# Kernel optimization log

Measured on AMD Instinct MI355X. Metric: run time of the kernel, lower is better.

## Reference

```python
import jax, jax.numpy as jnp
import numpy as np

B, N, C = 4, 2048, 1024
H = 16
HD = C // H
SCALE = HD ** -0.5


def setup_inputs() -> dict:
    key = jax.random.key(0)
    ks = jax.random.split(key, 5)
    s = 0.02
    return {
        "x": jax.random.normal(ks[0], (B, N, C), dtype=jnp.float32),
        "w_qkv": jax.random.normal(ks[1], (C, 3 * C), dtype=jnp.float32) * s,
        "b_qkv": jnp.zeros((3 * C,), dtype=jnp.float32),
        "w_proj": jax.random.normal(ks[2], (C, C), dtype=jnp.float32) * s,
        "b_proj": jnp.zeros((C,), dtype=jnp.float32),
    }


def reference(x, w_qkv, b_qkv, w_proj, b_proj):
    b, n, c = x.shape
    qkv = x @ w_qkv + b_qkv                       # [b, n, 3c]
    qkv = qkv.reshape(b, n, 3, H, HD)
    qkv = jnp.transpose(qkv, (2, 0, 3, 1, 4))     # [3, b, h, n, hd]
    q, k, v = qkv[0], qkv[1], qkv[2]
    attn = jnp.einsum("bhqd,bhkd->bhqk", q, k) * SCALE
    attn = jax.nn.softmax(attn, axis=-1)
    out = jnp.einsum("bhqk,bhkd->bhqd", attn, v)  # [b, h, n, hd]
    out = jnp.transpose(out, (0, 2, 1, 3)).reshape(b, n, c)
    return out @ w_proj + b_proj
```

## Files before the change

kernel.cpp:

```cpp
#include <hip/hip_runtime.h>
#include <cstdint>
#include <cstddef>


typedef __attribute__((ext_vector_type(8))) short short8;
typedef __attribute__((ext_vector_type(4))) float f32x4;
typedef _Float16 half4 __attribute__((ext_vector_type(4)));

#if __has_builtin(__builtin_amdgcn_exp2f)
#define EXP2F(x) __builtin_amdgcn_exp2f(x)
#else
#define EXP2F(x) __expf((x) * 0.69314718056f)
#endif

__device__ __forceinline__ short f2bf(float x) {
  unsigned u = __builtin_bit_cast(unsigned, x);
  u += 0x7fffu + ((u >> 16) & 1u);
  return (short)(u >> 16);
}

__device__ __forceinline__ unsigned pkh(float a, float b) {
  auto h = __builtin_amdgcn_cvt_pkrtz(a, b);
  return __builtin_bit_cast(unsigned, h);
}

__device__ __forceinline__ void async16(const void* g, void* l) {
  __builtin_amdgcn_global_load_lds(
      (const __attribute__((address_space(1))) unsigned*)g,
      (__attribute__((address_space(3))) unsigned*)l, 16, 0, 0);
}

__device__ __forceinline__ void barrier_raw() {
  __asm__ volatile("" ::: "memory");
  __builtin_amdgcn_s_barrier();
  __asm__ volatile("" ::: "memory");
}


__global__ __launch_bounds__(256) void prep_kernel(
    const float* __restrict__ x, const float* __restrict__ w_qkv,
    const float* __restrict__ w_proj, short* __restrict__ xs,
    short* __restrict__ wqkvT, short* __restrict__ wprojT) {
  __shared__ float tile[32][33];
  const int bid = blockIdx.x, tid = threadIdx.x;
  if (bid < 4096) {
    int i = bid * 256 + tid;
    const float4* p = (const float4*)x + (size_t)i * 2;
    float4 a = p[0], b = p[1];
    short8 r;
    r[0] = f2bf(a.x); r[1] = f2bf(a.y); r[2] = f2bf(a.z); r[3] = f2bf(a.w);
    r[4] = f2bf(b.x); r[5] = f2bf(b.y); r[6] = f2bf(b.z); r[7] = f2bf(b.w);
    *((short8*)xs + i) = r;
    return;
  }
  const float* in;
  short* out;
  int N, bx, by;
  if (bid < 4096 + 3072) {
    int b = bid - 4096;
    in = w_qkv; out = wqkvT; N = 3072; bx = b % 96; by = b / 96;
  } else {
    int b = bid - 7168;
    in = w_proj; out = wprojT; N = 1024; bx = b & 31; by = b >> 5;
  }
  const int K = 1024;
  int n0 = bx * 32, k0 = by * 32;
  int tx = tid & 31, ty = tid >> 5;
  for (int r = ty; r < 32; r += 8)
    tile[r][tx] = in[(size_t)(k0 + r) * N + n0 + tx];
  __syncthreads();
  for (int r = ty; r < 32; r += 8)
    out[(size_t)(n0 + r) * K + k0 + tx] = f2bf(tile[tx][r]);
}


template <int BM, int BN, int MODE>
__global__ __launch_bounds__(256, 2) void gemm_kernel(
    const short* __restrict__ A, const short* __restrict__ Bt,
    const float* __restrict__ bias, int Nn,
    short* __restrict__ qb, short* __restrict__ kb, short* __restrict__ vtb,
    float* __restrict__ outp) {
  constexpr int K = 1024;
  constexpr int NT = K / 32;
  constexpr int MR = BM / 32, NR = BN / 32;
  constexpr int L = (BM + BN) / 64;
  __shared__ __align__(16) short Ts[3][(BM + BN) * 32];
  const int tid = threadIdx.x, wave = tid >> 6, lane = tid & 63;
  const int quad = lane >> 4, l16 = lane & 15;

  const unsigned bid = blockIdx.x + gridDim.x * blockIdx.y;
  const unsigned c = bid & 7u, j = bid >> 3;
  const unsigned MC = gridDim.y >> 3;
  const unsigned chunk = MC * 8u;
  const unsigned nc = j / chunk, rem = j - nc * chunk;
  const unsigned m_idx = c * MC + (rem >> 3);
  const unsigned n_idx = nc * 8u + (rem & 7u);
  const int m0 = (int)m_idx * BM, n0 = (int)n_idx * BN;

  const int wrow = (wave >> 1) * (BM / 2), wcol = (wave & 1) * (BN / 2);

  const int srow = tid >> 2;
  const int sch8 = (((tid & 3) ^ (srow & 3)) * 8);
  const short* Ag = A + (size_t)(m0 + srow) * K + sch8;
  const short* Bg = Bt + (size_t)(n0 + srow) * K + sch8;
  const int fq8 = ((quad ^ (l16 & 3)) * 8);

  f32x4 acc[MR][NR] = {};

  auto stage = [&](int b, int kt) {
    char* dst = (char*)Ts[b] + tid * 16;
#pragma unroll
    for (int i = 0; i < BM / 64; ++i)
      async16(Ag + (size_t)(i * 64) * K + kt * 32, dst + i * 4096);
#pragma unroll
    for (int i = 0; i < BN / 64; ++i)
      async16(Bg + (size_t)(i * 64) * K + kt * 32, dst + (BM / 64 + i) * 4096);
  };

  stage(0, 0);
  stage(1, 1);
  if constexpr (L == 6) asm volatile("s_waitcnt vmcnt(6)" ::: "memory");
  else                  asm volatile("s_waitcnt vmcnt(4)" ::: "memory");
  barrier_raw();

  int cb = 0, sb = 2;
  for (int t = 0; t < NT; ++t) {
    if (t + 2 < NT) stage(sb, t + 2);

    const short* Tb = Ts[cb];
    short8 af[MR], bf[NR];
#pragma unroll
    for (int mf = 0; mf < MR; ++mf)
      af[mf] = *(const short8*)&Tb[(wrow + mf * 16 + l16) * 32 + fq8];
#pragma unroll
    for (int nf = 0; nf < NR; ++nf)
      bf[nf] = *(const short8*)&Tb[(BM + wcol + nf * 16 + l16) * 32 + fq8];

    __builtin_amdgcn_s_setprio(1);
#pragma unroll
    for (int mf = 0; mf < MR; ++mf)
#pragma unroll
      for (int nf = 0; nf < NR; ++nf)
        acc[mf][nf] = __builtin_amdgcn_mfma_f32_16x16x32_bf16(
            af[mf], bf[nf], acc[mf][nf], 0, 0, 0);
    __builtin_amdgcn_s_setprio(0);

    if (t + 2 < NT) {
      if constexpr (L == 6) asm volatile("s_waitcnt vmcnt(6)" ::: "memory");
      else                  asm volatile("s_waitcnt vmcnt(4)" ::: "memory");
    } else {
      asm volatile("s_waitcnt vmcnt(0)" ::: "memory");
    }
    barrier_raw();
    cb = cb + 1; if (cb >= 3) cb -= 3;
    sb = sb + 1; if (sb >= 3) sb -= 3;
  }

  if (MODE == 0) {
#pragma unroll
    for (int mf = 0; mf < MR; ++mf) {
      int row0 = m0 + wrow + mf * 16 + quad * 4;
      int b = row0 >> 11, n = row0 & 2047;
#pragma unroll
      for (int nf = 0; nf < NR; ++nf) {
        int col = n0 + wcol + nf * 16 + l16;
        float bv = bias[col];
        float v0 = acc[mf][nf][0] + bv, v1 = acc[mf][nf][1] + bv;
        float v2 = acc[mf][nf][2] + bv, v3 = acc[mf][nf][3] + bv;
        int which = col >> 10;
        int h = (col >> 6) & 15;
        int d = col & 63;
        size_t bh = (size_t)(b * 16 + h);
        if (which == 0) {
          const float qs = 0.18033688f;
          size_t base = (bh * 2048 + n) * 64 + d;
          qb[base]       = f2bf(v0 * qs);
          qb[base + 64]  = f2bf(v1 * qs);
          qb[base + 128] = f2bf(v2 * qs);
          qb[base + 192] = f2bf(v3 * qs);
        } else if (which == 1) {
          size_t base = (bh * 2048 + n) * 64 + d;
          kb[base]       = f2bf(v0);
          kb[base + 64]  = f2bf(v1);
          kb[base + 128] = f2bf(v2);
          kb[base + 192] = f2bf(v3);
        } else {
          uint2 pk;
          pk.x = pkh(v0, v1);
          pk.y = pkh(v2, v3);
          *(uint2*)&vtb[(bh * 64 + d) * 2048 + n] = pk;
        }
      }
    }
  } else {
#pragma unroll
    for (int mf = 0; mf < MR; ++mf) {
      int row0 = m0 + wrow + mf * 16 + quad * 4;
#pragma unroll
      for (int nf = 0; nf < NR; ++nf) {
        int col = n0 + wcol + nf * 16 + l16;
        float bv = bias[col];
        outp[(size_t)row0 * Nn + col]       = acc[mf][nf][0] + bv;
        outp[(size_t)(row0 + 1) * Nn + col] = acc[mf][nf][1] + bv;
        outp[(size_t)(row0 + 2) * Nn + col] = acc[mf][nf][2] + bv;
        outp[(size_t)(row0 + 3) * Nn + col] = acc[mf][nf][3] + bv;
      }
    }
  }
}


__global__ __launch_bounds__(256, 4) void attn_kernel(
    const short* __restrict__ qb, const short* __restrict__ kb,
    const short* __restrict__ vtb, short* __restrict__ ob) {
  __shared__ __align__(16) short Ks[2][64 * 64];
  __shared__ __align__(16) short Vs[2][64 * 64];
  const int tid = threadIdx.x, wave = tid >> 6, lane = tid & 63;
  const int quad = lane >> 4, l16 = lane & 15;
  int nlin = blockIdx.x + blockIdx.y * 16;
  nlin = (nlin & 7) * 128 + (nlin >> 3);
  const int q0 = (nlin & 15) * 128;
  const int bh = nlin >> 4;
  const short* Qg = qb + (size_t)bh * (2048 * 64);
  const short* Kg = kb + (size_t)bh * (2048 * 64);
  const short* Vg = vtb + (size_t)bh * (64 * 2048);

  short8 qf[2][2];
#pragma unroll
  for (int qt = 0; qt < 2; ++qt)
#pragma unroll
    for (int kc = 0; kc < 2; ++kc)
      qf[qt][kc] = *(const short8*)
          &Qg[(size_t)(q0 + wave * 32 + qt * 16 + l16) * 64 + kc * 32 + quad * 8];

  const int str = lane >> 3;
  const int sgc = ((lane & 7) ^ (str & 7)) * 8;
  const int fsw = l16 & 7;
  const int c0 = wave * 2, c1 = wave * 2 + 1;

  async16(Kg + (size_t)(c0 * 8 + str) * 64 + sgc, (char*)Ks[0] + c0 * 1024);
  async16(Kg + (size_t)(c1 * 8 + str) * 64 + sgc, (char*)Ks[0] + c1 * 1024);
  async16(Vg + (size_t)(c0 * 8 + str) * 2048 + sgc, (char*)Vs[0] + c0 * 1024);
  async16(Vg + (size_t)(c1 * 8 + str) * 2048 + sgc, (char*)Vs[0] + c1 * 1024);

  const half4 vone = {(_Float16)1.f, (_Float16)1.f, (_Float16)1.f, (_Float16)1.f};
  const f32x4 fz = {};
  f32x4 oacc[2][4] = {};
  f32x4 lacc[2] = {};

  for (int t = 0; t < 32; ++t) {
    __syncthreads();

    int kvn = (t + 1) * 64;
    if (kvn < 2048) {
      char* kd = (char*)Ks[(t + 1) & 1];
      char* vd = (char*)Vs[(t + 1) & 1];
      async16(Kg + (size_t)(kvn + c0 * 8 + str) * 64 + sgc, kd + c0 * 1024);
      async16(Kg + (size_t)(kvn + c1 * 8 + str) * 64 + sgc, kd + c1 * 1024);
      async16(Vg + (size_t)(c0 * 8 + str) * 2048 + kvn + sgc, vd + c0 * 1024);
      async16(Vg + (size_t)(c1 * 8 + str) * 2048 + kvn + sgc, vd + c1 * 1024);
    }
    const short* Kst = Ks[t & 1];
    const short* Vst = Vs[t & 1];

    f32x4 sacc[2][4];
#pragma unroll
    for (int kc = 0; kc < 2; ++kc) {
      short8 kf[4];
#pragma unroll
      for (int kvt = 0; kvt < 4; ++kvt)
        kf[kvt] = *(const short8*)
            &Kst[(kvt * 16 + l16) * 64 + (((kc * 4 + quad) ^ fsw) << 3)];
#pragma unroll
      for (int kvt = 0; kvt < 4; ++kvt)
#pragma unroll
        for (int qt = 0; qt < 2; ++qt)
          sacc[qt][kvt] = __builtin_amdgcn_mfma_f32_16x16x32_bf16(
              kf[kvt], qf[qt][kc], kc == 0 ? fz : sacc[qt][kvt], 0, 0, 0);
    }

#pragma unroll
    for (int kvt = 0; kvt < 4; ++kvt) {
      const int vcol = (((kvt * 2 + (quad >> 1)) ^ fsw) << 3) + (quad & 1) * 4;
      uint2 vr[4];
#pragma unroll
      for (int nt = 0; nt < 4; ++nt)
        vr[nt] = *(const uint2*)&Vst[(nt * 16 + l16) * 64 + vcol];

      half4 pfr[2];
#pragma unroll
      for (int qt = 0; qt < 2; ++qt) {
        float p0 = EXP2F(sacc[qt][kvt][0]);
        float p1 = EXP2F(sacc[qt][kvt][1]);
        float p2 = EXP2F(sacc[qt][kvt][2]);
        float p3 = EXP2F(sacc[qt][kvt][3]);
        uint2 w;
        w.x = pkh(p0, p1);
        w.y = pkh(p2, p3);
        pfr[qt] = __builtin_bit_cast(half4, w);
      }
#pragma unroll
      for (int qt = 0; qt < 2; ++qt)
        lacc[qt] = __builtin_amdgcn_mfma_f32_16x16x16f16(
            pfr[qt], vone, lacc[qt], 0, 0, 0);
#pragma unroll
      for (int nt = 0; nt < 4; ++nt) {
        half4 vfr = __builtin_bit_cast(half4, vr[nt]);
#pragma unroll
        for (int qt = 0; qt < 2; ++qt)
          oacc[qt][nt] = __builtin_amdgcn_mfma_f32_16x16x16f16(
              pfr[qt], vfr, oacc[qt][nt], 0, 0, 0);
      }
    }
  }

  const int b = bh >> 4, h = bh & 15;
#pragma unroll
  for (int qt = 0; qt < 2; ++qt) {
    float inv0 = 1.f / lacc[qt][0], inv1 = 1.f / lacc[qt][1];
    float inv2 = 1.f / lacc[qt][2], inv3 = 1.f / lacc[qt][3];
#pragma unroll
    for (int nt = 0; nt < 4; ++nt) {
      int d = nt * 16 + l16;
      int qbase = q0 + wave * 32 + qt * 16 + quad * 4;
      size_t obase = ((size_t)(b * 2048 + qbase)) * 1024 + h * 64 + d;
      ob[obase]        = f2bf(oacc[qt][nt][0] * inv0);
      ob[obase + 1024] = f2bf(oacc[qt][nt][1] * inv1);
      ob[obase + 2048] = f2bf(oacc[qt][nt][2] * inv2);
      ob[obase + 3072] = f2bf(oacc[qt][nt][3] * inv3);
    }
  }
}


extern "C" void kernel_launch(void* const* d_in, const int* in_sizes, int n_in,
                              void* d_out, int out_size, void* d_ws, size_t ws_size,
                              hipStream_t stream) {
  const float* x      = (const float*)d_in[0];
  const float* w_qkv  = (const float*)d_in[1];
  const float* b_qkv  = (const float*)d_in[2];
  const float* w_proj = (const float*)d_in[3];
  const float* b_proj = (const float*)d_in[4];
  float* out = (float*)d_out;

  short* xs     = (short*)d_ws;
  short* wqkvT  = xs + (size_t)8192 * 1024;
  short* wprojT = wqkvT + (size_t)3072 * 1024;
  short* qb     = wprojT + (size_t)1024 * 1024;
  short* kb     = qb + (size_t)64 * 2048 * 64;
  short* vtb    = kb + (size_t)64 * 2048 * 64;
  short* aob    = vtb + (size_t)64 * 2048 * 64;

  prep_kernel<<<dim3(8192), 256, 0, stream>>>(x, w_qkv, w_proj,
                                              xs, wqkvT, wprojT);

  gemm_kernel<256, 128, 0><<<dim3(24, 32), 256, 0, stream>>>(
      xs, wqkvT, b_qkv, 3072, qb, kb, vtb, nullptr);
  attn_kernel<<<dim3(16, 64), 256, 0, stream>>>(qb, kb, vtb, aob);
  gemm_kernel<128, 128, 1><<<dim3(8, 64), 256, 0, stream>>>(
      aob, wprojT, b_proj, 1024, nullptr, nullptr, nullptr, out);
}
```

Measured before the change: 267.1 us.

## Switch attention kernel to 32x32 MFMA tiles with permlane32 P-fragment swap

Rewrites the attention inner loop to use 32x32x16 MFMA instructions for both QK^T and PV, so each wave holds 32 query rows in lane-indexed layout. The softmax row sum is now accumulated directly in registers instead of through an extra MFMA against a ones vector. The P fragments are rearranged across wave halves with permlane32_swap, and s_setprio is raised around the PV MFMAs. This aims to cut MFMA instruction count, LDS reads and the redundant sum MFMAs, at the cost of a more complex register layout and a cross-lane shuffle.

```diff
diff --git a/kernel.cpp b/kernel.cpp
--- a/kernel.cpp
+++ b/kernel.cpp
@@ -5,7 +5,9 @@
 
 typedef __attribute__((ext_vector_type(8))) short short8;
 typedef __attribute__((ext_vector_type(4))) float f32x4;
-typedef _Float16 half4 __attribute__((ext_vector_type(4)));
+typedef __attribute__((ext_vector_type(16))) float f32x16;
+typedef _Float16 half8 __attribute__((ext_vector_type(8)));
+typedef __attribute__((ext_vector_type(2))) int iv2;
 
 #if __has_builtin(__builtin_amdgcn_exp2f)
 #define EXP2F(x) __builtin_amdgcn_exp2f(x)
@@ -216,7 +218,7 @@
   __shared__ __align__(16) short Ks[2][64 * 64];
   __shared__ __align__(16) short Vs[2][64 * 64];
   const int tid = threadIdx.x, wave = tid >> 6, lane = tid & 63;
-  const int quad = lane >> 4, l16 = lane & 15;
+  const int l31 = lane & 31, hi = lane >> 5;
   int nlin = blockIdx.x + blockIdx.y * 16;
   nlin = (nlin & 7) * 128 + (nlin >> 3);
   const int q0 = (nlin & 15) * 128;
@@ -225,17 +227,14 @@
   const short* Kg = kb + (size_t)bh * (2048 * 64);
   const short* Vg = vtb + (size_t)bh * (64 * 2048);
 
-  short8 qf[2][2];
-#pragma unroll
-  for (int qt = 0; qt < 2; ++qt)
-#pragma unroll
-    for (int kc = 0; kc < 2; ++kc)
-      qf[qt][kc] = *(const short8*)
-          &Qg[(size_t)(q0 + wave * 32 + qt * 16 + l16) * 64 + kc * 32 + quad * 8];
+  const int qrow = q0 + wave * 32 + l31;
+  short8 qf[4];
+#pragma unroll
+  for (int ds = 0; ds < 4; ++ds)
+    qf[ds] = *(const short8*)&Qg[(size_t)qrow * 64 + ds * 16 + hi * 8];
 
   const int str = lane >> 3;
   const int sgc = ((lane & 7) ^ (str & 7)) * 8;
-  const int fsw = l16 & 7;
   const int c0 = wave * 2, c1 = wave * 2 + 1;
 
   async16(Kg + (size_t)(c0 * 8 + str) * 64 + sgc, (char*)Ks[0] + c0 * 1024);
@@ -243,10 +242,9 @@
   async16(Vg + (size_t)(c0 * 8 + str) * 2048 + sgc, (char*)Vs[0] + c0 * 1024);
   async16(Vg + (size_t)(c1 * 8 + str) * 2048 + sgc, (char*)Vs[0] + c1 * 1024);
 
-  const half4 vone = {(_Float16)1.f, (_Float16)1.f, (_Float16)1.f, (_Float16)1.f};
-  const f32x4 fz = {};
-  f32x4 oacc[2][4] = {};
-  f32x4 lacc[2] = {};
+  const f32x16 fz16 = {};
+  f32x16 oacc[2] = {};
+  float dsum = 0.f;
 
   for (int t = 0; t < 32; ++t) {
     __syncthreads();
@@ -263,73 +261,74 @@
     const short* Kst = Ks[t & 1];
     const short* Vst = Vs[t & 1];
 
-    f32x4 sacc[2][4];
-#pragma unroll
-    for (int kc = 0; kc < 2; ++kc) {
-      short8 kf[4];
-#pragma unroll
-      for (int kvt = 0; kvt < 4; ++kvt)
-        kf[kvt] = *(const short8*)
-            &Kst[(kvt * 16 + l16) * 64 + (((kc * 4 + quad) ^ fsw) << 3)];
-#pragma unroll
-      for (int kvt = 0; kvt < 4; ++kvt)
-#pragma unroll
-        for (int qt = 0; qt < 2; ++qt)
-          sacc[qt][kvt] = __builtin_amdgcn_mfma_f32_16x16x32_bf16(
-              kf[kvt], qf[qt][kc], kc == 0 ? fz : sacc[qt][kvt], 0, 0, 0);
-    }
-
-#pragma unroll
-    for (int kvt = 0; kvt < 4; ++kvt) {
-      const int vcol = (((kvt * 2 + (quad >> 1)) ^ fsw) << 3) + (quad & 1) * 4;
-      uint2 vr[4];
-#pragma unroll
-      for (int nt = 0; nt < 4; ++nt)
-        vr[nt] = *(const uint2*)&Vst[(nt * 16 + l16) * 64 + vcol];
-
-      half4 pfr[2];
-#pragma unroll
-      for (int qt = 0; qt < 2; ++qt) {
-        float p0 = EXP2F(sacc[qt][kvt][0]);
-        float p1 = EXP2F(sacc[qt][kvt][1]);
-        float p2 = EXP2F(sacc[qt][kvt][2]);
-        float p3 = EXP2F(sacc[qt][kvt][3]);
-        uint2 w;
-        w.x = pkh(p0, p1);
-        w.y = pkh(p2, p3);
-        pfr[qt] = __builtin_bit_cast(half4, w);
-      }
-#pragma unroll
-      for (int qt = 0; qt < 2; ++qt)
-        lacc[qt] = __builtin_amdgcn_mfma_f32_16x16x16f16(
-            pfr[qt], vone, lacc[qt], 0, 0, 0);
-#pragma unroll
-      for (int nt = 0; nt < 4; ++nt) {
-        half4 vfr = __builtin_bit_cast(half4, vr[nt]);
-#pragma unroll
-        for (int qt = 0; qt < 2; ++qt)
-          oacc[qt][nt] = __builtin_amdgcn_mfma_f32_16x16x16f16(
-              pfr[qt], vfr, oacc[qt][nt], 0, 0, 0);
-      }
-    }
-  }
-
+    f32x16 sacc[2];
+#pragma unroll
+    for (int blk = 0; blk < 2; ++blk) {
+      const int row = blk * 32 + l31;
+      const int key = row & 7;
+#pragma unroll
+      for (int ds = 0; ds < 4; ++ds) {
+        short8 kfr = *(const short8*)
+            &Kst[row * 64 + (((ds * 2 + hi) ^ key) << 3)];
+        sacc[blk] = __builtin_amdgcn_mfma_f32_32x32x16_bf16(
+            kfr, qf[ds], ds == 0 ? fz16 : sacc[blk], 0, 0, 0);
+      }
+    }
+
+#pragma unroll
+    for (int blk = 0; blk < 2; ++blk) {
+      unsigned w[8];
+#pragma unroll
+      for (int i = 0; i < 8; ++i) {
+        float p0 = EXP2F(sacc[blk][2 * i]);
+        float p1 = EXP2F(sacc[blk][2 * i + 1]);
+        dsum += p0 + p1;
+        w[i] = pkh(p0, p1);
+      }
+      half8 pf[2];
+#pragma unroll
+      for (int s = 0; s < 2; ++s) {
+        iv2 r1 = __builtin_amdgcn_permlane32_swap(
+            (int)w[4 * s + 0], (int)w[4 * s + 2], false, false);
+        iv2 r2 = __builtin_amdgcn_permlane32_swap(
+            (int)w[4 * s + 1], (int)w[4 * s + 3], false, false);
+        uint4 u;
+        u.x = (unsigned)r1[0];
+        u.y = (unsigned)r2[0];
+        u.z = (unsigned)r1[1];
+        u.w = (unsigned)r2[1];
+        pf[s] = __builtin_bit_cast(half8, u);
+      }
+      __builtin_amdgcn_s_setprio(1);
+#pragma unroll
+      for (int s = 0; s < 2; ++s) {
+        const int kvs = blk * 2 + s;
+#pragma unroll
+        for (int db = 0; db < 2; ++db) {
+          const int vrow = db * 32 + l31;
+          half8 vf = *(const half8*)
+              &Vst[vrow * 64 + (((kvs * 2 + hi) ^ (vrow & 7)) << 3)];
+          oacc[db] = __builtin_amdgcn_mfma_f32_32x32x16_f16(
+              vf, pf[s], oacc[db], 0, 0, 0);
+        }
+      }
+      __builtin_amdgcn_s_setprio(0);
+    }
+  }
+
+  dsum += __shfl_xor(dsum, 32, 64);
+  const float inv = 1.f / dsum;
   const int b = bh >> 4, h = bh & 15;
-#pragma unroll
-  for (int qt = 0; qt < 2; ++qt) {
-    float inv0 = 1.f / lacc[qt][0], inv1 = 1.f / lacc[qt][1];
-    float inv2 = 1.f / lacc[qt][2], inv3 = 1.f / lacc[qt][3];
-#pragma unroll
-    for (int nt = 0; nt < 4; ++nt) {
-      int d = nt * 16 + l16;
-      int qbase = q0 + wave * 32 + qt * 16 + quad * 4;
-      size_t obase = ((size_t)(b * 2048 + qbase)) * 1024 + h * 64 + d;
-      ob[obase]        = f2bf(oacc[qt][nt][0] * inv0);
-      ob[obase + 1024] = f2bf(oacc[qt][nt][1] * inv1);
-      ob[obase + 2048] = f2bf(oacc[qt][nt][2] * inv2);
-      ob[obase + 3072] = f2bf(oacc[qt][nt][3] * inv3);
-    }
-  }
+  const size_t rowbase = ((size_t)(b * 2048 + qrow)) * 1024 + h * 64;
+#pragma unroll
+  for (int db = 0; db < 2; ++db)
+#pragma unroll
+    for (int i = 0; i < 8; ++i) {
+      const int d0 = ((2 * i) & 3) + 8 * (i >> 1) + 4 * hi + 32 * db;
+      unsigned s0 = (unsigned short)f2bf(oacc[db][2 * i] * inv);
+      unsigned s1 = (unsigned short)f2bf(oacc[db][2 * i + 1] * inv);
+      *(unsigned*)&ob[rowbase + d0] = s0 | (s1 << 16);
+    }
 }
 
 
```

New measurement: 268.9 us. About the same (+0.7%).
